# Performance work log

Hardware: AMD Instinct MI355X
Metric: run time of the kernel (lower is better)

The kernel has to match this reference:

```python
import jax, jax.numpy as jnp
from jax import lax
import numpy as np

MAX_ITER = 200      # hard-coded in DyanEncoder.forward
N_REWEIGHT = 3      # outer reweighting rounds
EPS_W = 0.01


def build_dictionary(rr, theta, T):
    # rows i=0..T-1: [1, rr^i*cos(i*th), (-rr)^i*cos(i*th), rr^i*sin(i*th), (-rr)^i*sin(i*th)]
    i = jnp.arange(T, dtype=rr.dtype)[:, None]          # [T,1]
    pow_p = jnp.power(rr[None, :], i)                   # rr^i, [T,N]
    sign = 1.0 - 2.0 * (jnp.arange(T) % 2).astype(rr.dtype)[:, None]
    pow_m = sign * pow_p                                # (-rr)^i
    c = jnp.cos(i * theta[None, :])
    s = jnp.sin(i * theta[None, :])
    ones = jnp.ones((T, 1), dtype=rr.dtype)
    return jnp.concatenate([ones, pow_p * c, pow_m * c, pow_p * s, pow_m * s], axis=1)  # [T, 1+4N]


def fista_reweighted(D, Y, lam, w):
    # D: [T,K], Y: [B,T,P], w: broadcastable to [B,K,P]
    DtD = D.T @ D                                       # [K,K]
    DtY = jnp.einsum('tk,btp->bkp', D, Y)               # [B,K,P]
    L = jnp.linalg.norm(DtD, ord=2)                     # spectral norm
    Linv = 1.0 / L
    # torch uses Linv.data.item() here -> detached scalar
    w_lam = w * lam * lax.stop_gradient(Linv)
    K = DtD.shape[1]
    A = jnp.eye(K, dtype=D.dtype) - DtD * Linv
    c_minus = DtY * Linv - w_lam
    c_plus = DtY * Linv + w_lam
    x0 = jnp.zeros_like(DtY)

    def step(carry, _):
        x_old, y_old, t_old = carry
        Ay = jnp.einsum('kj,bjp->bkp', A, y_old)
        x_new = jnp.maximum(0.0, Ay + c_minus) + jnp.minimum(0.0, Ay + c_plus)
        t_new = (1.0 + jnp.sqrt(1.0 + 4.0 * t_old ** 2)) / 2.0
        y_new = x_new + ((t_old - 1.0) / t_new) * (x_new - x_old)
        return (x_new, y_new, t_new), None

    (x_fin, _, _), _ = lax.scan(step, (x0, x0, jnp.float32(1.0)), None, length=MAX_ITER)
    return x_fin


def setup_inputs() -> dict:
    key = jax.random.key(0)
    k1, k2, k3 = jax.random.split(key, 3)
    Npoles = 160
    B, T, P = 1, 36, 512
    x = jax.random.normal(k1, (B, T, P), dtype=jnp.float32)
    rr = jax.random.uniform(k2, (Npoles,), dtype=jnp.float32)            # pole magnitudes in (0,1)
    theta = jax.random.uniform(k3, (Npoles,), dtype=jnp.float32) * 3.1415927  # pole angles
    return {"x": x, "rr": rr, "theta": theta, "T": T}


def reference(x, rr, theta, T):
    lam = 0.1
    dic = build_dictionary(rr, theta, T)                # [T, K]
    K = dic.shape[1]
    B, _, P = x.shape
    w = jnp.ones((1, K, P), dtype=x.dtype)
    final = None
    for _ in range(N_REWEIGHT):
        temp = fista_reweighted(dic, x, lam, w)         # [B,K,P]
        wr = 1.0 / (jnp.abs(temp) + EPS_W)
        w = wr / jnp.linalg.norm(wr.reshape(-1))
        final = temp
    return final, dic
```

## Files before the change

kernel.cpp:

```cpp
#include <hip/hip_runtime.h>
#include <math.h>

#define TT 36
#define NP 160
#define KDIM 641
#define PP 512
#define KPAD 704
#define ZERO_SLOT 664
#define DUMP_SLOT 672
#define NU 321
#define BT 512
#define LAM 0.1f
#define EPSW 0.01f
#define NITER 200
#define NPOW 160

__global__ void k_build_dic(const float* __restrict__ rr, const float* __restrict__ th,
                            float* __restrict__ D, float* __restrict__ outD) {
  int idx = blockIdx.x * blockDim.x + threadIdx.x;
  if (idx >= TT * KDIM) return;
  int t = idx / KDIM, k = idx % KDIM;
  float v;
  if (k == 0) {
    v = 1.0f;
  } else {
    int g = (k - 1) / NP;
    int p = (k - 1) % NP;
    float ft = (float)t;
    float pw = powf(rr[p], ft);
    if ((g == 1 || g == 3) && (t & 1)) pw = -pw;
    float ang = ft * th[p];
    v = pw * ((g < 2) ? cosf(ang) : sinf(ang));
  }
  D[idx] = v;
  outD[idx] = v;
}

__global__ void k_G(const float* __restrict__ D, float* __restrict__ G) {
  int idx = blockIdx.x * blockDim.x + threadIdx.x;
  if (idx >= TT * TT) return;
  int i = idx / TT, j = idx % TT;
  float s = 0.0f;
  for (int k = 0; k < KDIM; ++k) s = fmaf(D[i * KDIM + k], D[j * KDIM + k], s);
  G[idx] = s;
}

__global__ void k_power(const float* __restrict__ G, float* __restrict__ Lb) {
  int lane = threadIdx.x;
  float g[TT];
#pragma unroll
  for (int j = 0; j < TT; ++j) g[j] = (lane < TT) ? G[lane * TT + j] : 0.0f;
  float v = (lane < TT) ? 1.0f : 0.0f;
  for (int it = 0; it < NPOW; ++it) {
    float u = 0.0f;
#pragma unroll
    for (int j = 0; j < TT; ++j) u = fmaf(g[j], __shfl(v, j, 64), u);
    float s = u * u;
#pragma unroll
    for (int o = 32; o >= 1; o >>= 1) s += __shfl_xor(s, o, 64);
    v = u * rsqrtf(s);
  }
  float u = 0.0f;
#pragma unroll
  for (int j = 0; j < TT; ++j) u = fmaf(g[j], __shfl(v, j, 64), u);
  float num = v * u, den = v * v;
#pragma unroll
  for (int o = 32; o >= 1; o >>= 1) {
    num += __shfl_xor(num, o, 64);
    den += __shfl_xor(den, o, 64);
  }
  if (lane == 0) {
    float L = num / den;
    Lb[0] = L;
    Lb[1] = 1.0f / L;
    Lb[3] = 0.0f;
  }
}

template <int C>
__device__ __forceinline__ float dppadd(float v) {
  int t = __builtin_amdgcn_update_dpp(0, __float_as_int(v), C, 0xf, 0xf, true);
  return v + __int_as_float(t);
}
__device__ __forceinline__ float wave_sum63(float v) {
  v = dppadd<0xB1>(v);
  v = dppadd<0x4E>(v);
  v = dppadd<0x141>(v);
  v = dppadd<0x140>(v);
  v = dppadd<0x142>(v);
  v = dppadd<0x143>(v);
  return v;
}

__device__ __forceinline__ void unit_map(int u, int& kP, int& kM) {
  if (u == 0)       { kP = 0;        kM = DUMP_SLOT; }
  else if (u < 161) { kP = u;        kM = u + 160; }
  else              { kP = u + 160;  kM = u + 320; }
}

__global__ __launch_bounds__(BT, 4) void k_round(
    const float* __restrict__ Dg, const float* __restrict__ X,
    float* __restrict__ Lb, const float* __restrict__ xprev,
    float* __restrict__ xout, int first, int last) {
  __shared__ __align__(16) float ylds[KPAD];
  __shared__ __align__(16) float zlds[40];

  const int tid  = threadIdx.x;
  const int lane = tid & 63;
  const int w    = tid >> 6;
  const int nr   = (w < 4) ? 5 : 4;
  const float sgn = (w & 1) ? -1.0f : 1.0f;
  const int p    = blockIdx.x;

  const float Linv = Lb[1];
  const float lamL = LAM * Linv;

  const int u = tid;
  const bool act = (u < NU);
  int kP, kM;
  unit_map(act ? u : 0, kP, kM);

  int kA[6], kB[6];
#pragma unroll
  for (int j = 0; j < 6; ++j) {
    const int ua = lane + 64 * j;
    int ka, kb;
    if (ua == 0)       { ka = 0;        kb = ZERO_SLOT; }
    else if (ua < 161) { ka = ua;       kb = ua + 160; }
    else if (ua < NU)  { ka = ua + 160; kb = ua + 320; }
    else               { ka = ZERO_SLOT; kb = ZERO_SLOT; }
    kA[j] = ka; kB[j] = kb;
  }

  float Dq[5][6];
#pragma unroll
  for (int i = 0; i < 5; ++i)
#pragma unroll
    for (int j = 0; j < 6; ++j) {
      const int ua = lane + 64 * j;
      Dq[i][j] = (i < nr && ua < NU) ? Dg[(w + 8 * i) * KDIM + kA[j]] : 0.0f;
    }

  float Dc[TT];
#pragma unroll
  for (int t = 0; t < TT; ++t) Dc[t] = act ? Dg[t * KDIM + kP] : 0.0f;

  float cmP, cpP, cmM, cpM;
  {
    float sE = 0.f, sO = 0.f;
#pragma unroll
    for (int t = 0; t < TT; ++t) {
      const float xv = X[t * PP + p];
      if (t & 1) sO = fmaf(Dc[t], xv, sO);
      else       sE = fmaf(Dc[t], xv, sE);
    }
    const float c0P = (sE + sO) * Linv, c0M = (sE - sO) * Linv;
    float wlP = lamL, wlM = lamL;
    if (!first) {
      const float nl = lamL * Lb[2];
      wlP = nl / (fabsf(xprev[p * KPAD + kP]) + EPSW);
      wlM = nl / (fabsf(xprev[p * KPAD + ((u > 0) ? kM : kP)]) + EPSW);
    }
    cmP = c0P - wlP; cpP = c0P + wlP;
    cmM = c0M - wlM; cpM = c0M + wlM;
  }

  for (int i = tid; i < KPAD; i += BT) ylds[i] = 0.0f;

  float xP = 0.f, xM = 0.f, yP = 0.f, yM = 0.f;
  float tmom = 1.0f;

  __syncthreads();

  for (int it = 0; it < NITER; ++it) {
    float acc[5];
#pragma unroll
    for (int i = 0; i < 5; ++i) acc[i] = 0.f;
#pragma unroll
    for (int j = 0; j < 6; ++j) {
      const float yA = ylds[kA[j]];
      const float yB = ylds[kB[j]];
      const float op = fmaf(sgn, yB, yA);
#pragma unroll
      for (int i = 0; i < 5; ++i) acc[i] = fmaf(Dq[i][j], op, acc[i]);
    }
#pragma unroll
    for (int i = 0; i < 5; ++i) {
      if (i < nr) {
        const float r = wave_sum63(acc[i]);
        if (lane == 63) zlds[w + 8 * i] = r * Linv;
      }
    }
    __syncthreads();

    const float tn = 0.5f * (1.0f + sqrtf(1.0f + 4.0f * tmom * tmom));
    const float mu = (tmom - 1.0f) / tn;
    tmom = tn;

    if (act) {
      float sE = 0.f, sO = 0.f;
#pragma unroll
      for (int q = 0; q < 9; ++q) {
        const float4 z4 = *reinterpret_cast<const float4*>(&zlds[4 * q]);
        sE = fmaf(Dc[4*q+0], z4.x, sE);
        sO = fmaf(Dc[4*q+1], z4.y, sO);
        sE = fmaf(Dc[4*q+2], z4.z, sE);
        sO = fmaf(Dc[4*q+3], z4.w, sO);
      }
      const float sP = sE + sO, sM = sE - sO;
      float uu, xn;
      uu = yP - sP; xn = fmaxf(0.f, uu + cmP) + fminf(0.f, uu + cpP);
      yP = fmaf(mu, xn - xP, xn); xP = xn;
      uu = yM - sM; xn = fmaxf(0.f, uu + cmM) + fminf(0.f, uu + cpM);
      yM = fmaf(mu, xn - xM, xn); xM = xn;
      ylds[kP] = yP;
      ylds[kM] = yM;
    }
    __syncthreads();
  }

  if (act) {
    if (last) {
      xout[kP * PP + p] = xP;
      if (u > 0) xout[kM * PP + p] = xM;
    } else {
      xout[p * KPAD + kP] = xP;
      if (u > 0) xout[p * KPAD + kM] = xM;
    }
  }

  if (!last) {
    float s = 0.0f;
    if (act) {
      const float rP = 1.0f / (fabsf(xP) + EPSW);
      s = rP * rP;
      if (u > 0) { const float rM = 1.0f / (fabsf(xM) + EPSW); s += rM * rM; }
    }
    s = wave_sum63(s);
    if (lane == 63) zlds[w] = s;
    __syncthreads();
    if (tid == 0) {
      float tot = 0.f;
#pragma unroll
      for (int i = 0; i < 8; ++i) tot += zlds[i];
      atomicAdd(&Lb[3], tot);
    }
  }
}

__global__ void k_norm(float* __restrict__ Lb) {
  if (threadIdx.x == 0) {
    Lb[2] = 1.0f / sqrtf(Lb[3]);
    Lb[3] = 0.0f;
  }
}

extern "C" void kernel_launch(void* const* d_in, const int* in_sizes, int n_in,
                              void* d_out, int out_size, void* d_ws, size_t ws_size,
                              hipStream_t stream) {
  const float* x  = (const float*)d_in[0];
  const float* rr = (const float*)d_in[1];
  const float* th = (const float*)d_in[2];
  float* out = (float*)d_out;
  float* ws  = (float*)d_ws;

  size_t off = 0;
  auto alloc = [&](size_t n) {
    float* p = ws + off;
    off += (n + 63) & ~(size_t)63;
    return p;
  };
  float* D    = alloc((size_t)TT * KDIM);
  float* G    = alloc(TT * TT);
  float* Lb   = alloc(16);
  float* xa   = alloc((size_t)PP * KPAD);
  if (off * sizeof(float) > ws_size) return;

  k_build_dic<<<(TT * KDIM + 255) / 256, 256, 0, stream>>>(rr, th, D, out + (size_t)KDIM * PP);
  k_G<<<(TT * TT + 255) / 256, 256, 0, stream>>>(D, G);
  k_power<<<1, 64, 0, stream>>>(G, Lb);

  for (int r = 0; r < 3; ++r) {
    const int first = (r == 0), last = (r == 2);
    float* xo = last ? out : xa;
    k_round<<<PP, BT, 0, stream>>>(D, x, Lb, xa, xo, first, last);
    if (!last) k_norm<<<1, 64, 0, stream>>>(Lb);
  }
}
```

Before: 821.3 us.

## Pack y pairs as float2 in LDS and precompute FISTA momentum table

Each unit's plus and minus y values are now stored interleaved as a float2 in shared memory, indexed by unit. The inner matvec therefore does one 64-bit LDS load per column instead of two scattered loads through index arrays, which also frees the kA/kB registers. The FISTA momentum coefficients are computed once in the power kernel and read from an LDS table, removing a sqrt and a divide from each iteration. Inline asm is added to keep the D coefficients pinned in registers, and occupancy attributes are set explicitly; both add dependence on compiler behaviour.

```diff
diff --git a/kernel.cpp b/kernel.cpp
--- a/kernel.cpp
+++ b/kernel.cpp
@@ -6,9 +6,8 @@
 #define KDIM 641
 #define PP 512
 #define KPAD 704
-#define ZERO_SLOT 664
-#define DUMP_SLOT 672
 #define NU 321
+#define YSLOTS 384
 #define BT 512
 #define LAM 0.1f
 #define EPSW 0.01f
@@ -45,7 +44,8 @@
   G[idx] = s;
 }
 
-__global__ void k_power(const float* __restrict__ G, float* __restrict__ Lb) {
+__global__ void k_power(const float* __restrict__ G, float* __restrict__ Lb,
+                        float* __restrict__ mug) {
   int lane = threadIdx.x;
   float g[TT];
 #pragma unroll
@@ -74,6 +74,12 @@
     Lb[0] = L;
     Lb[1] = 1.0f / L;
     Lb[3] = 0.0f;
+    float t = 1.0f;
+    for (int i = 0; i < NITER; ++i) {
+      float tn = 0.5f * (1.0f + sqrtf(1.0f + 4.0f * t * t));
+      mug[i] = (t - 1.0f) / tn;
+      t = tn;
+    }
   }
 }
 
@@ -92,18 +98,19 @@
   return v;
 }
 
-__device__ __forceinline__ void unit_map(int u, int& kP, int& kM) {
-  if (u == 0)       { kP = 0;        kM = DUMP_SLOT; }
-  else if (u < 161) { kP = u;        kM = u + 160; }
-  else              { kP = u + 160;  kM = u + 320; }
-}
-
-__global__ __launch_bounds__(BT, 4) void k_round(
+__device__ __forceinline__ int colmap(int u) {
+  return (u == 0) ? 0 : ((u < 161) ? u : u + 160);
+}
+
+__global__ __attribute__((amdgpu_flat_work_group_size(BT, BT), amdgpu_waves_per_eu(4, 4)))
+void k_round(
     const float* __restrict__ Dg, const float* __restrict__ X,
-    float* __restrict__ Lb, const float* __restrict__ xprev,
-    float* __restrict__ xout, int first, int last) {
-  __shared__ __align__(16) float ylds[KPAD];
+    float* __restrict__ Lb, const float* __restrict__ mug,
+    const float* __restrict__ xprev, float* __restrict__ xout,
+    int first, int last) {
+  __shared__ __align__(16) float2 ylds2[YSLOTS];
   __shared__ __align__(16) float zlds[40];
+  __shared__ float muLDS[NITER];
 
   const int tid  = threadIdx.x;
   const int lane = tid & 63;
@@ -117,20 +124,8 @@
 
   const int u = tid;
   const bool act = (u < NU);
-  int kP, kM;
-  unit_map(act ? u : 0, kP, kM);
-
-  int kA[6], kB[6];
-#pragma unroll
-  for (int j = 0; j < 6; ++j) {
-    const int ua = lane + 64 * j;
-    int ka, kb;
-    if (ua == 0)       { ka = 0;        kb = ZERO_SLOT; }
-    else if (ua < 161) { ka = ua;       kb = ua + 160; }
-    else if (ua < NU)  { ka = ua + 160; kb = ua + 320; }
-    else               { ka = ZERO_SLOT; kb = ZERO_SLOT; }
-    kA[j] = ka; kB[j] = kb;
-  }
+  const int kP = colmap(act ? u : 0);
+  const int kM = (u == 0 || !act) ? 0 : kP + 160;
 
   float Dq[5][6];
 #pragma unroll
@@ -138,12 +133,20 @@
 #pragma unroll
     for (int j = 0; j < 6; ++j) {
       const int ua = lane + 64 * j;
-      Dq[i][j] = (i < nr && ua < NU) ? Dg[(w + 8 * i) * KDIM + kA[j]] : 0.0f;
-    }
+      Dq[i][j] = (i < nr && ua < NU) ? Dg[(w + 8 * i) * KDIM + colmap(ua)] : 0.0f;
+    }
+#pragma unroll
+  for (int i = 0; i < 5; ++i)
+#pragma unroll
+    for (int j = 0; j < 6; ++j)
+      asm volatile("v_mov_b32 %0, %0" : "+v"(Dq[i][j]));
 
   float Dc[TT];
 #pragma unroll
   for (int t = 0; t < TT; ++t) Dc[t] = act ? Dg[t * KDIM + kP] : 0.0f;
+#pragma unroll
+  for (int t = 0; t < TT; ++t)
+    asm volatile("v_mov_b32 %0, %0" : "+v"(Dc[t]));
 
   float cmP, cpP, cmM, cpM;
   {
@@ -165,10 +168,10 @@
     cmM = c0M - wlM; cpM = c0M + wlM;
   }
 
-  for (int i = tid; i < KPAD; i += BT) ylds[i] = 0.0f;
+  if (tid < NITER) muLDS[tid] = mug[tid];
+  if (tid < YSLOTS) ylds2[tid] = make_float2(0.f, 0.f);
 
   float xP = 0.f, xM = 0.f, yP = 0.f, yM = 0.f;
-  float tmom = 1.0f;
 
   __syncthreads();
 
@@ -178,9 +181,8 @@
     for (int i = 0; i < 5; ++i) acc[i] = 0.f;
 #pragma unroll
     for (int j = 0; j < 6; ++j) {
-      const float yA = ylds[kA[j]];
-      const float yB = ylds[kB[j]];
-      const float op = fmaf(sgn, yB, yA);
+      const float2 yv = ylds2[lane + 64 * j];
+      const float op = fmaf(sgn, yv.y, yv.x);
 #pragma unroll
       for (int i = 0; i < 5; ++i) acc[i] = fmaf(Dq[i][j], op, acc[i]);
     }
@@ -193,10 +195,7 @@
     }
     __syncthreads();
 
-    const float tn = 0.5f * (1.0f + sqrtf(1.0f + 4.0f * tmom * tmom));
-    const float mu = (tmom - 1.0f) / tn;
-    tmom = tn;
-
+    const float mu = muLDS[it];
     if (act) {
       float sE = 0.f, sO = 0.f;
 #pragma unroll
@@ -213,8 +212,8 @@
       yP = fmaf(mu, xn - xP, xn); xP = xn;
       uu = yM - sM; xn = fmaxf(0.f, uu + cmM) + fminf(0.f, uu + cpM);
       yM = fmaf(mu, xn - xM, xn); xM = xn;
-      ylds[kP] = yP;
-      ylds[kM] = yM;
+      const float yMs = (u == 0) ? 0.0f : yM;
+      ylds2[u] = make_float2(yP, yMs);
     }
     __syncthreads();
   }
@@ -273,17 +272,18 @@
   float* D    = alloc((size_t)TT * KDIM);
   float* G    = alloc(TT * TT);
   float* Lb   = alloc(16);
+  float* mug  = alloc(NITER);
   float* xa   = alloc((size_t)PP * KPAD);
   if (off * sizeof(float) > ws_size) return;
 
   k_build_dic<<<(TT * KDIM + 255) / 256, 256, 0, stream>>>(rr, th, D, out + (size_t)KDIM * PP);
   k_G<<<(TT * TT + 255) / 256, 256, 0, stream>>>(D, G);
-  k_power<<<1, 64, 0, stream>>>(G, Lb);
+  k_power<<<1, 64, 0, stream>>>(G, Lb, mug);
 
   for (int r = 0; r < 3; ++r) {
     const int first = (r == 0), last = (r == 2);
     float* xo = last ? out : xa;
-    k_round<<<PP, BT, 0, stream>>>(D, x, Lb, xa, xo, first, last);
+    k_round<<<PP, BT, 0, stream>>>(D, x, Lb, mug, xa, xo, first, last);
     if (!last) k_norm<<<1, 64, 0, stream>>>(Lb);
   }
 }
```

Measured after the change: 728.7 us. -11.3%, faster.
